# Performance work log

Measured on AMD Instinct MI355X. Metric: run time of the kernel, lower is better.

The kernel has to match this reference:

```python
import jax, jax.numpy as jnp
import numpy as np

N = 512          # data_info['n']
K = 513          # data_info['k'] + 1
B = 65536        # batch size


def _build_adjust(n, k):
    # Reproduces the __init__ mask construction exactly.
    a1 = np.ones((n - 1, k - 1, 2), dtype=np.float32)
    a2 = np.zeros((n - 1, k - 1, 2), dtype=np.float32)
    for i in range(0, k - 2):
        if i >= n - 1:
            break
        f1 = a1[i].reshape(-1)
        f1[2 + 2 * i:] = 0
        a1[i] = f1.reshape(k - 1, 2)
        f2 = a2[i].reshape(-1)
        f2[2 + 2 * i + 1] = 1
        a2[i] = f2.reshape(k - 1, 2)
    return jnp.asarray(a1), jnp.asarray(a2)


W_ADJ1, W_ADJ2 = _build_adjust(N, K)


def setup_inputs() -> dict:
    key = jax.random.key(0)
    k1, k2, k3 = jax.random.split(key, 3)
    x = jax.random.randint(k1, (B, N), 0, 2, dtype=jnp.int32)
    W = jax.random.normal(k2, (N - 1, K - 1, 2), dtype=jnp.float32)
    endW = jax.random.normal(k3, (1, K), dtype=jnp.float32)
    return {"x": x, "W": W, "endW": endW}


def reference(x, W, endW):
    # W_full construction (softmax over the 2-way split, masked, with the
    # deterministic [1,0] row prepended along the group axis).
    Wsm = jax.nn.softmax(W, axis=2)                      # (n-1, k-1, 2)
    W_full = Wsm * W_ADJ1 + W_ADJ2                       # (n-1, k-1, 2)
    append = jnp.zeros((N - 1, 1, 2), W_full.dtype).at[:, :, 0].set(1.0)
    W_full = jnp.concatenate([append, W_full], axis=1)   # (n-1, k, 2)

    # group_num at step i is the running cumsum of x[:, 0..i]; the serial
    # recurrence collapses to a single cumsum, letting us gather all steps
    # at once instead of the original n-1 step Python loop.
    g = jnp.cumsum(x, axis=1)                            # (B, n)
    steps = jnp.arange(N - 1)                            # step i -> W_full[i-1]
    vals = W_full[steps[None, :], g[:, 1:], x[:, 1:]]    # (B, n-1)
    out = jnp.sum(jnp.log(vals), axis=1, keepdims=True)  # (B, 1)

    e = jax.nn.softmax(endW, axis=1)[0]                  # (k,)
    out = out + jnp.log(e[g[:, -1]])[:, None]            # (B, 1)
    return out
```

## Files before the change

### kernel.cpp

```cpp
#include <hip/hip_runtime.h>
#include <math.h>

#define NN      512
#define KK      513
#define BB      65536
#define TROWS   512
#define TCOLS   513
#define T16STR  528

#define RPB     64
#define NSEG    8
#define SEGW    64
#define BLK     (RPB * NSEG)
#define XSTR    129

typedef int iv4 __attribute__((ext_vector_type(4)));

__device__ __forceinline__ unsigned f2bf(float f) {
    unsigned u = __float_as_uint(f);
    return (u + 0x7fffu + ((u >> 16) & 1u)) >> 16;
}

__global__ void build_table_kernel(const float* __restrict__ W, unsigned* __restrict__ T16) {
    int idx = blockIdx.x * blockDim.x + threadIdx.x;
    if (idx >= TROWS * TCOLS) return;
    int t = idx / TCOLS;
    int g = idx - t * TCOLS;
    float v0 = 0.f, v1 = 0.f;
    if (t >= 1 && g >= 1 && g <= t) {
        const float* w = W + ((size_t)(t - 1) * (KK - 1) + (g - 1)) * 2;
        float w0 = w[0], w1 = w[1];
        float m  = fmaxf(w0, w1);
        float lse = m + logf(expf(w0 - m) + expf(w1 - m));
        v0 = w0 - lse;
        v1 = w1 - lse;
    }
    T16[t * T16STR + g] = f2bf(v0) | (f2bf(v1) << 16);
}

__global__ void build_endw_kernel(const float* __restrict__ endW, float* __restrict__ logE) {
    int lane = threadIdx.x;
    float vals[9];
    float m = -1e30f;
    #pragma unroll
    for (int k = 0; k < 9; ++k) {
        int i = lane + 64 * k;
        vals[k] = (i < KK) ? endW[i] : -1e30f;
        m = fmaxf(m, vals[k]);
    }
    #pragma unroll
    for (int d = 32; d >= 1; d >>= 1) m = fmaxf(m, __shfl_xor(m, d, 64));
    float s = 0.f;
    #pragma unroll
    for (int k = 0; k < 9; ++k) s += expf(vals[k] - m);
    #pragma unroll
    for (int d = 32; d >= 1; d >>= 1) s += __shfl_xor(s, d, 64);
    float lse = m + logf(s);
    #pragma unroll
    for (int k = 0; k < 9; ++k) {
        int i = lane + 64 * k;
        if (i < KK) logE[i] = endW[i] - lse;
    }
}

__global__ __launch_bounds__(BLK, 8) void pc_main_kernel(
    const int* __restrict__ x, const unsigned* __restrict__ T16,
    const float* __restrict__ logE, float* __restrict__ out)
{
    __shared__ unsigned xb[RPB * XSTR];
    __shared__ int      segsum[NSEG * RPB];
    __shared__ float    partial[NSEG * RPB];

    const int tid  = threadIdx.x;
    const int row0 = blockIdx.x * RPB;

    {
        const iv4* tile = (const iv4*)(x + (size_t)row0 * NN);
        #pragma unroll
        for (int j = 0; j < 16; ++j) {
            int i = tid + BLK * j;
            iv4 a = tile[i];
            unsigned m = (unsigned)(a.x & 1) | ((unsigned)(a.y & 1) << 8)
                       | ((unsigned)(a.z & 1) << 16) | ((unsigned)(a.w & 1) << 24);
            xb[(i >> 7) * XSTR + (i & 127)] = m;
        }
    }
    __syncthreads();

    const int seg  = tid >> 6;
    const int lane = tid & 63;

    unsigned w[16];
    int ssum = 0;
    #pragma unroll
    for (int m = 0; m < 16; ++m) {
        w[m] = xb[lane * XSTR + seg * 16 + m];
        ssum += __popc(w[m]);
    }
    segsum[seg * 64 + lane] = ssum;
    __syncthreads();

    int g = 0, gtot = 0;
    #pragma unroll
    for (int s = 0; s < NSEG; ++s) {
        int v = segsum[s * 64 + lane];
        if (s < seg) g += v;
        gtot += v;
    }

    float a0 = 0.f, a1 = 0.f, a2 = 0.f, a3 = 0.f;
    const unsigned* Tseg = T16 + (size_t)(seg * SEGW) * T16STR;
    #pragma unroll
    for (int m = 0; m < 16; ++m) {
        const unsigned* Tm = Tseg + (size_t)(4 * m) * T16STR;
        unsigned wm = w[m];
        int b0 = wm & 1;         g += b0; unsigned u0 = Tm[0 * T16STR + g];
        a0 += __uint_as_float(b0 ? (u0 & 0xffff0000u) : (u0 << 16));
        int b1 = (wm >> 8)  & 1; g += b1; unsigned u1 = Tm[1 * T16STR + g];
        a1 += __uint_as_float(b1 ? (u1 & 0xffff0000u) : (u1 << 16));
        int b2 = (wm >> 16) & 1; g += b2; unsigned u2 = Tm[2 * T16STR + g];
        a2 += __uint_as_float(b2 ? (u2 & 0xffff0000u) : (u2 << 16));
        int b3 = (wm >> 24) & 1; g += b3; unsigned u3 = Tm[3 * T16STR + g];
        a3 += __uint_as_float(b3 ? (u3 & 0xffff0000u) : (u3 << 16));
    }
    partial[seg * 64 + lane] = (a0 + a1) + (a2 + a3);
    __syncthreads();

    if (seg == 0) {
        float s = logE[gtot];
        #pragma unroll
        for (int t = 0; t < NSEG; ++t) s += partial[t * 64 + lane];
        out[row0 + lane] = s;
    }
}

extern "C" void kernel_launch(void* const* d_in, const int* in_sizes, int n_in,
                              void* d_out, int out_size, void* d_ws, size_t ws_size,
                              hipStream_t stream)
{
    const int*   x    = (const int*)d_in[0];
    const float* W    = (const float*)d_in[1];
    const float* endW = (const float*)d_in[2];
    float*       out  = (float*)d_out;

    unsigned* T16  = (unsigned*)d_ws;
    float*    logE = (float*)((char*)d_ws + (size_t)TROWS * T16STR * sizeof(unsigned));

    {
        int total  = TROWS * TCOLS;
        int blocks = (total + 255) / 256;
        build_table_kernel<<<blocks, 256, 0, stream>>>(W, T16);
    }
    build_endw_kernel<<<1, 64, 0, stream>>>(endW, logE);
    pc_main_kernel<<<BB / RPB, BLK, 0, stream>>>(x, T16, logE, out);
}
```

Before: 214.9 us.

## Restructure main kernel to per-wave row groups with shuffle scans

The main kernel now gives each wave 8 rows, splitting each row across 8 segments. It packs x bits into nibbles with nontemporal loads, transposes them through a small per-wave shared buffer, and does the segment prefix sum and final reduction with wave shuffles. This removes the block-wide syncthreads and the larger shared-memory staging. The endW softmax is folded into the table-build kernel to save a launch, and the transcendentals now use fast intrinsics. The risks are less latency hiding from 32-step serial gather chains per thread, and a reliance on sched_barrier instead of a real barrier for the intra-wave shared-memory exchange.

```diff
diff --git a/kernel.cpp b/kernel.cpp
--- a/kernel.cpp
+++ b/kernel.cpp
@@ -8,11 +8,7 @@
 #define TCOLS   513
 #define T16STR  528
 
-#define RPB     64
-#define NSEG    8
-#define SEGW    64
-#define BLK     (RPB * NSEG)
-#define XSTR    129
+#define BLK     256
 
 typedef int iv4 __attribute__((ext_vector_type(4)));
 
@@ -21,45 +17,46 @@
     return (u + 0x7fffu + ((u >> 16) & 1u)) >> 16;
 }
 
-__global__ void build_table_kernel(const float* __restrict__ W, unsigned* __restrict__ T16) {
+__global__ void build_table_kernel(const float* __restrict__ W, const float* __restrict__ endW,
+                                   unsigned* __restrict__ T16, float* __restrict__ logE) {
     int idx = blockIdx.x * blockDim.x + threadIdx.x;
-    if (idx >= TROWS * TCOLS) return;
-    int t = idx / TCOLS;
-    int g = idx - t * TCOLS;
-    float v0 = 0.f, v1 = 0.f;
-    if (t >= 1 && g >= 1 && g <= t) {
-        const float* w = W + ((size_t)(t - 1) * (KK - 1) + (g - 1)) * 2;
-        float w0 = w[0], w1 = w[1];
-        float m  = fmaxf(w0, w1);
-        float lse = m + logf(expf(w0 - m) + expf(w1 - m));
-        v0 = w0 - lse;
-        v1 = w1 - lse;
+    if (idx < TROWS * TCOLS) {
+        int t = idx / TCOLS;
+        int g = idx - t * TCOLS;
+        float v0 = 0.f, v1 = 0.f;
+        if (t >= 1 && g >= 1 && g <= t) {
+            const float* w = W + ((size_t)(t - 1) * (KK - 1) + (g - 1)) * 2;
+            float w0 = w[0], w1 = w[1];
+            float m  = fmaxf(w0, w1);
+            float lse = m + __logf(__expf(w0 - m) + __expf(w1 - m));
+            v0 = w0 - lse;
+            v1 = w1 - lse;
+        }
+        T16[t * T16STR + g] = f2bf(v0) | (f2bf(v1) << 16);
     }
-    T16[t * T16STR + g] = f2bf(v0) | (f2bf(v1) << 16);
-}
-
-__global__ void build_endw_kernel(const float* __restrict__ endW, float* __restrict__ logE) {
-    int lane = threadIdx.x;
-    float vals[9];
-    float m = -1e30f;
-    #pragma unroll
-    for (int k = 0; k < 9; ++k) {
-        int i = lane + 64 * k;
-        vals[k] = (i < KK) ? endW[i] : -1e30f;
-        m = fmaxf(m, vals[k]);
-    }
-    #pragma unroll
-    for (int d = 32; d >= 1; d >>= 1) m = fmaxf(m, __shfl_xor(m, d, 64));
-    float s = 0.f;
-    #pragma unroll
-    for (int k = 0; k < 9; ++k) s += expf(vals[k] - m);
-    #pragma unroll
-    for (int d = 32; d >= 1; d >>= 1) s += __shfl_xor(s, d, 64);
-    float lse = m + logf(s);
-    #pragma unroll
-    for (int k = 0; k < 9; ++k) {
-        int i = lane + 64 * k;
-        if (i < KK) logE[i] = endW[i] - lse;
+    if (blockIdx.x == 0 && threadIdx.x < 64) {
+        int lane = threadIdx.x;
+        float vals[9];
+        float m = -1e30f;
+        #pragma unroll
+        for (int k = 0; k < 9; ++k) {
+            int i = lane + 64 * k;
+            vals[k] = (i < KK) ? endW[i] : -1e30f;
+            m = fmaxf(m, vals[k]);
+        }
+        #pragma unroll
+        for (int d = 32; d >= 1; d >>= 1) m = fmaxf(m, __shfl_xor(m, d, 64));
+        float s = 0.f;
+        #pragma unroll
+        for (int k = 0; k < 9; ++k) s += __expf(vals[k] - m);
+        #pragma unroll
+        for (int d = 32; d >= 1; d >>= 1) s += __shfl_xor(s, d, 64);
+        float lse = m + __logf(s);
+        #pragma unroll
+        for (int k = 0; k < 9; ++k) {
+            int i = lane + 64 * k;
+            if (i < KK) logE[i] = endW[i] - lse;
+        }
     }
 }
 
@@ -67,71 +64,86 @@
     const int* __restrict__ x, const unsigned* __restrict__ T16,
     const float* __restrict__ logE, float* __restrict__ out)
 {
-    __shared__ unsigned xb[RPB * XSTR];
-    __shared__ int      segsum[NSEG * RPB];
-    __shared__ float    partial[NSEG * RPB];
+    __shared__ unsigned xposed[4 * 128];
 
     const int tid  = threadIdx.x;
-    const int row0 = blockIdx.x * RPB;
+    const int wid  = tid >> 6;
+    const int lane = tid & 63;
+    const int gw   = blockIdx.x * 4 + wid;
+    const int ridx = lane & 7;
+    const int s    = lane >> 3;
 
+    const iv4* xt = (const iv4*)(x + (size_t)gw * (8 * NN));
+    unsigned p0 = 0, p1 = 0;
     {
-        const iv4* tile = (const iv4*)(x + (size_t)row0 * NN);
+        iv4 A[8];
         #pragma unroll
-        for (int j = 0; j < 16; ++j) {
-            int i = tid + BLK * j;
-            iv4 a = tile[i];
-            unsigned m = (unsigned)(a.x & 1) | ((unsigned)(a.y & 1) << 8)
-                       | ((unsigned)(a.z & 1) << 16) | ((unsigned)(a.w & 1) << 24);
-            xb[(i >> 7) * XSTR + (i & 127)] = m;
+        for (int j = 0; j < 8; ++j) A[j] = __builtin_nontemporal_load(&xt[j * 64 + lane]);
+        #pragma unroll
+        for (int j = 0; j < 8; ++j) {
+            unsigned nib = (unsigned)(A[j].x & 1) | ((unsigned)(A[j].y & 1) << 1)
+                         | ((unsigned)(A[j].z & 1) << 2) | ((unsigned)(A[j].w & 1) << 3);
+            p0 |= nib << (4 * j);
+        }
+        #pragma unroll
+        for (int j = 0; j < 8; ++j) A[j] = __builtin_nontemporal_load(&xt[(8 + j) * 64 + lane]);
+        #pragma unroll
+        for (int j = 0; j < 8; ++j) {
+            unsigned nib = (unsigned)(A[j].x & 1) | ((unsigned)(A[j].y & 1) << 1)
+                         | ((unsigned)(A[j].z & 1) << 2) | ((unsigned)(A[j].w & 1) << 3);
+            p1 |= nib << (4 * j);
         }
     }
-    __syncthreads();
 
-    const int seg  = tid >> 6;
-    const int lane = tid & 63;
+    unsigned* wb = &xposed[wid * 128];
+    wb[lane]      = p0;
+    wb[64 + lane] = p1;
+    __builtin_amdgcn_sched_barrier(0);
 
-    unsigned w[16];
-    int ssum = 0;
+    const unsigned base  = ((ridx < 4) ? 0u : 64u) + 16u * (s & 3);
+    const int      shift = 4 * ((2 * ridx + (s >> 2)) & 7);
+    unsigned lo = 0, hi = 0;
     #pragma unroll
-    for (int m = 0; m < 16; ++m) {
-        w[m] = xb[lane * XSTR + seg * 16 + m];
-        ssum += __popc(w[m]);
+    for (int m = 0; m < 8; ++m)  lo |= ((wb[base + m] >> shift) & 0xFu) << (4 * m);
+    #pragma unroll
+    for (int m = 8; m < 16; ++m) hi |= ((wb[base + m] >> shift) & 0xFu) << (4 * (m - 8));
+
+    int pc  = __popc(lo) + __popc(hi);
+    int inc = pc, t1;
+    t1 = __shfl_up(inc, 8,  64); if (s >= 1) inc += t1;
+    t1 = __shfl_up(inc, 16, 64); if (s >= 2) inc += t1;
+    t1 = __shfl_up(inc, 32, 64); if (s >= 4) inc += t1;
+    int g = inc - pc;
+
+    float a0 = 0.f, a1 = 0.f, a2 = 0.f, a3 = 0.f;
+    const unsigned* Ts = T16 + (size_t)(64 * s) * T16STR;
+    #pragma unroll
+    for (int k = 0; k < 32; ++k) {
+        int b = (lo >> k) & 1; g += b;
+        unsigned u = Ts[k * T16STR + g];
+        float v = __uint_as_float(b ? (u & 0xffff0000u) : (u << 16));
+        if      ((k & 3) == 0) a0 += v;
+        else if ((k & 3) == 1) a1 += v;
+        else if ((k & 3) == 2) a2 += v;
+        else                   a3 += v;
     }
-    segsum[seg * 64 + lane] = ssum;
-    __syncthreads();
-
-    int g = 0, gtot = 0;
     #pragma unroll
-    for (int s = 0; s < NSEG; ++s) {
-        int v = segsum[s * 64 + lane];
-        if (s < seg) g += v;
-        gtot += v;
+    for (int k = 0; k < 32; ++k) {
+        int b = (hi >> k) & 1; g += b;
+        unsigned u = Ts[(32 + k) * T16STR + g];
+        float v = __uint_as_float(b ? (u & 0xffff0000u) : (u << 16));
+        if      ((k & 3) == 0) a0 += v;
+        else if ((k & 3) == 1) a1 += v;
+        else if ((k & 3) == 2) a2 += v;
+        else                   a3 += v;
     }
 
-    float a0 = 0.f, a1 = 0.f, a2 = 0.f, a3 = 0.f;
-    const unsigned* Tseg = T16 + (size_t)(seg * SEGW) * T16STR;
-    #pragma unroll
-    for (int m = 0; m < 16; ++m) {
-        const unsigned* Tm = Tseg + (size_t)(4 * m) * T16STR;
-        unsigned wm = w[m];
-        int b0 = wm & 1;         g += b0; unsigned u0 = Tm[0 * T16STR + g];
-        a0 += __uint_as_float(b0 ? (u0 & 0xffff0000u) : (u0 << 16));
-        int b1 = (wm >> 8)  & 1; g += b1; unsigned u1 = Tm[1 * T16STR + g];
-        a1 += __uint_as_float(b1 ? (u1 & 0xffff0000u) : (u1 << 16));
-        int b2 = (wm >> 16) & 1; g += b2; unsigned u2 = Tm[2 * T16STR + g];
-        a2 += __uint_as_float(b2 ? (u2 & 0xffff0000u) : (u2 << 16));
-        int b3 = (wm >> 24) & 1; g += b3; unsigned u3 = Tm[3 * T16STR + g];
-        a3 += __uint_as_float(b3 ? (u3 & 0xffff0000u) : (u3 << 16));
-    }
-    partial[seg * 64 + lane] = (a0 + a1) + (a2 + a3);
-    __syncthreads();
-
-    if (seg == 0) {
-        float s = logE[gtot];
-        #pragma unroll
-        for (int t = 0; t < NSEG; ++t) s += partial[t * 64 + lane];
-        out[row0 + lane] = s;
-    }
+    float part = (a0 + a1) + (a2 + a3);
+    part += __shfl_xor(part, 8,  64);
+    part += __shfl_xor(part, 16, 64);
+    part += __shfl_xor(part, 32, 64);
+    if (s == 7)
+        out[gw * 8 + ridx] = part + logE[inc];
 }
 
 extern "C" void kernel_launch(void* const* d_in, const int* in_sizes, int n_in,
@@ -148,9 +160,8 @@
 
     {
         int total  = TROWS * TCOLS;
-        int blocks = (total + 255) / 256;
-        build_table_kernel<<<blocks, 256, 0, stream>>>(W, T16);
+        int blocks = (total + BLK - 1) / BLK;
+        build_table_kernel<<<blocks, BLK, 0, stream>>>(W, endW, T16, logE);
     }
-    build_endw_kernel<<<1, 64, 0, stream>>>(endW, logE);
-    pc_main_kernel<<<BB / RPB, BLK, 0, stream>>>(x, T16, logE, out);
+    pc_main_kernel<<<BB / (8 * 4), BLK, 0, stream>>>(x, T16, logE, out);
 }
```

Result: no change. 211.3 us (-1.7%).
